# Optimization experiments

Hardware: AMD Instinct MI355X
Metric: run time of the kernel (lower is better)

The kernel has to match this reference:

```python
import jax, jax.numpy as jnp
import numpy as np

B_, N_, H_ = 4, 256, 32          # batch, nodes, neighbors (edges = B*N*H)
NC_IN, NC_OUT = 16, 16
NUM_FREQ, D_OUT, M_IN = 3, 3, 3  # degree_in = degree_out = 1 -> 2*1+1
EDGE_DIM, HID = 16, 64
LN_EPS = 1e-5


def _ln(x, gamma):
    # torch F.layer_norm over last dim, beta fixed at zero
    mu = jnp.mean(x, axis=-1, keepdims=True)
    var = jnp.var(x, axis=-1, keepdims=True)
    return (x - mu) * jax.lax.rsqrt(var + LN_EPS) * gamma


def setup_inputs() -> dict:
    key = jax.random.key(0)
    ks = jax.random.split(key, 8)

    def lin(k, fin, fout):
        lim = 1.0 / np.sqrt(fin)
        kw, kb = jax.random.split(k)
        W = jax.random.uniform(kw, (fin, fout), jnp.float32, -lim, lim)
        b = jax.random.uniform(kb, (fout,), jnp.float32, -lim, lim)
        return W, b

    W1, b1 = lin(ks[0], EDGE_DIM + 1, HID)
    W2, b2 = lin(ks[1], HID, HID)
    W3, b3 = lin(ks[2], HID, NUM_FREQ * NC_IN * NC_OUT)
    return {
        "feat": jax.random.normal(ks[3], (B_, N_, H_, EDGE_DIM + 1), jnp.float32),
        "basis": jax.random.normal(ks[4], (B_, N_, H_, D_OUT, M_IN, NUM_FREQ), jnp.float32),
        "W1": W1, "b1": b1, "g1": jnp.ones((HID,), jnp.float32),
        "W2": W2, "b2": b2, "g2": jnp.ones((HID,), jnp.float32),
        "W3": W3, "b3": b3,
    }


def reference(feat, basis, W1, b1, g1, W2, b2, g2, W3, b3):
    # radial MLP: Linear -> SiLU -> LN -> Linear -> SiLU -> LN -> Linear
    h = _ln(jax.nn.silu(feat @ W1 + b1), g1)
    h = _ln(jax.nn.silu(h @ W2 + b2), g2)
    r = h @ W3 + b3                                   # (b, n, k, o*i*f)
    R = r.reshape(*r.shape[:-1], NC_OUT, NC_IN, NUM_FREQ)  # '(o i f) -> o i f'
    # per-frequency multiply-accumulate: sum_f R[...,o,i,f] * B[...,d,m,f]
    out = jnp.einsum('bnkoif,bnkdmf->bnkodim', R, basis)   # (b,n,k,o,d,i,m)
    b, n, k = out.shape[:3]
    # contiguous reshape matches torch rearrange + view: (b,n,k, d_out*nc_out, nc_in*m_in)
    return out.reshape(b, n, k, NC_OUT * D_OUT, NC_IN * M_IN)
```

## Files before the change

kernel.cpp:

```cpp
#include <hip/hip_runtime.h>

#define E_TOTAL 32768
#define F_IN 17
#define HID 64
#define NJ 768

using bf16x8 = __attribute__((ext_vector_type(8))) short;
using f32x4  = __attribute__((ext_vector_type(4))) float;

__device__ __forceinline__ unsigned short f2bf(float x){
    unsigned u = __float_as_uint(x);
    u += 0x7fffu + ((u >> 16) & 1u);
    return (unsigned short)(u >> 16);
}

__device__ __forceinline__ float wave_sum(float x){
    x += __int_as_float(__builtin_amdgcn_update_dpp(0, __float_as_int(x), 0x111, 0xf, 0xf, true));
    x += __int_as_float(__builtin_amdgcn_update_dpp(0, __float_as_int(x), 0x112, 0xf, 0xf, true));
    x += __int_as_float(__builtin_amdgcn_update_dpp(0, __float_as_int(x), 0x114, 0xf, 0xf, true));
    x += __int_as_float(__builtin_amdgcn_update_dpp(0, __float_as_int(x), 0x118, 0xf, 0xf, true));
    x += __int_as_float(__builtin_amdgcn_update_dpp(0, __float_as_int(x), 0x142, 0xa, 0xf, true));
    x += __int_as_float(__builtin_amdgcn_update_dpp(0, __float_as_int(x), 0x143, 0xc, 0xf, true));
    return __int_as_float(__builtin_amdgcn_readlane(__float_as_int(x), 63));
}

__global__ __launch_bounds__(256) void prep_w3(const float* __restrict__ W3,
                                               unsigned short* __restrict__ w3t){
    int t = blockIdx.x * 256 + threadIdx.x;
    int n = t >> 6, k = t & 63;
    w3t[t] = f2bf(W3[k * NJ + n]);
}

__global__ __launch_bounds__(256, 3) void fused_kernel(const float* __restrict__ feat,
        const float* __restrict__ W1, const float* __restrict__ b1, const float* __restrict__ g1,
        const float* __restrict__ W2, const float* __restrict__ b2, const float* __restrict__ g2,
        const unsigned short* __restrict__ w3t, const float* __restrict__ b3,
        const float* __restrict__ basis, float* __restrict__ out){
    __shared__ __align__(16) char smem[51968];
    unsigned short* sH  = (unsigned short*)smem;
    char* rgn = smem + 2304;
    float* sW1 = (float*)rgn;
    float* sW2 = (float*)(rgn + 4352);
    float* sC  = (float*)(rgn + 20736);
    float* sFe = (float*)(rgn + 21760);
    float* sH1 = (float*)(rgn + 22848);
    float* sR  = (float*)rgn;
    float* sO  = (float*)(rgn + 12544);

    int tid = threadIdx.x;
    int e0  = blockIdx.x * 16;
    int wv = tid >> 6, l = tid & 63;
    int j = l;
    int col = l & 15, kg = l >> 4;
    int e_loc = wv * 4 + kg;
    int s = col;

    for (int i = tid; i < 272; i += 256) ((f32x4*)sW1)[i] = ((const f32x4*)W1)[i];
    #pragma unroll
    for (int k = 0; k < 4; ++k) ((f32x4*)sW2)[k * 256 + tid] = ((const f32x4*)W2)[k * 256 + tid];
    if (tid < 64){
        int g = tid >> 4, r = tid & 15;
        const float* src = (g == 0) ? b1 : (g == 1) ? g1 : (g == 2) ? b2 : g2;
        ((f32x4*)sC)[tid] = ((const f32x4*)src)[r];
    }
    if (tid < 68) ((f32x4*)sFe)[tid] = ((const f32x4*)(feat + (size_t)e0 * F_IN))[tid];
    __syncthreads();

    float acc[4], x[4];

    #pragma unroll
    for (int q = 0; q < 4; ++q) acc[q] = sC[j];
    for (int k = 0; k < F_IN; ++k){
        float w = sW1[k * 64 + j];
        #pragma unroll
        for (int q = 0; q < 4; ++q) acc[q] += sFe[(wv * 4 + q) * F_IN + k] * w;
    }
    #pragma unroll
    for (int q = 0; q < 4; ++q){
        float a = acc[q];
        float sg = 1.0f / (1.0f + __expf(-a));
        x[q] = a * sg;
        float s1 = wave_sum(x[q]);
        float s2 = wave_sum(x[q] * x[q]);
        float mu  = s1 * (1.0f / 64.0f);
        float var = s2 * (1.0f / 64.0f) - mu * mu;
        float rs  = rsqrtf(var + 1e-5f);
        sH1[(wv * 4 + q) * 64 + j] = (x[q] - mu) * rs * sC[64 + j];
    }

    #pragma unroll
    for (int q = 0; q < 4; ++q) acc[q] = sC[128 + j];
    for (int k4 = 0; k4 < 16; ++k4){
        float hv[4][4];
        #pragma unroll
        for (int q = 0; q < 4; ++q) *(float4*)hv[q] = *(const float4*)&sH1[(wv * 4 + q) * 64 + k4 * 4];
        #pragma unroll
        for (int kk = 0; kk < 4; ++kk){
            float w = sW2[(k4 * 4 + kk) * 64 + j];
            #pragma unroll
            for (int q = 0; q < 4; ++q) acc[q] += hv[q][kk] * w;
        }
    }
    #pragma unroll
    for (int q = 0; q < 4; ++q){
        float a = acc[q];
        float sg = 1.0f / (1.0f + __expf(-a));
        x[q] = a * sg;
        float s1 = wave_sum(x[q]);
        float s2 = wave_sum(x[q] * x[q]);
        float mu  = s1 * (1.0f / 64.0f);
        float var = s2 * (1.0f / 64.0f) - mu * mu;
        float rs  = rsqrtf(var + 1e-5f);
        sH[(wv * 4 + q) * 72 + j] = f2bf((x[q] - mu) * rs * sC[192 + j]);
    }

    float bs[27];
    {
        const float* bp = basis + (size_t)(e0 + e_loc) * 27;
        #pragma unroll
        for (int z = 0; z < 27; ++z) bs[z] = bp[z];
    }
    __syncthreads();

    bf16x8 a0 = *(const bf16x8*)(sH + col * 72 + kg * 8);
    bf16x8 a1 = *(const bf16x8*)(sH + col * 72 + 32 + kg * 8);

    float* outB = out + (size_t)e0 * 2304;
    const float* Rrow = sR + e_loc * 196;
    float* Orow = sO + e_loc * 580;

    for (int c4 = 0; c4 < 4; ++c4){
        if (c4 > 0){
            #pragma unroll
            for (int k = 0; k < 9; ++k){
                int idx4 = k * 256 + tid;
                int e = idx4 / 144, c = idx4 - e * 144;
                f32x4 v = *(const f32x4*)(sO + e * 580 + c * 4);
                *(f32x4*)(outB + (size_t)e * 2304 + (c4 - 1) * 576 + c * 4) = v;
            }
        }
        #pragma unroll
        for (int t = 0; t < 3; ++t){
            int n0 = c4 * 192 + wv * 48 + t * 16;
            const unsigned short* wrow = w3t + (size_t)(n0 + col) * 64;
            bf16x8 bb0 = *(const bf16x8*)(wrow + kg * 8);
            bf16x8 bb1 = *(const bf16x8*)(wrow + 32 + kg * 8);
            f32x4 acc2 = {0.f, 0.f, 0.f, 0.f};
            acc2 = __builtin_amdgcn_mfma_f32_16x16x32_bf16(a0, bb0, acc2, 0, 0, 0);
            acc2 = __builtin_amdgcn_mfma_f32_16x16x32_bf16(a1, bb1, acc2, 0, 0, 0);
            float bj = b3[n0 + col];
            int cL = wv * 48 + t * 16 + col;
            #pragma unroll
            for (int r = 0; r < 4; ++r)
                sR[(kg * 4 + r) * 196 + cL] = acc2[r] + bj;
        }
        __syncthreads();

        #pragma unroll
        for (int t2 = 0; t2 < 4; ++t2){
            const float* rp = Rrow + t2 * 48 + s * 3;
            float r0 = rp[0], r1 = rp[1], r2 = rp[2];
            #pragma unroll
            for (int d = 0; d < 3; ++d){
                float* p = Orow + t2 * 144 + d * 48 + s * 3;
                int z = d * 9;
                p[0] = r0 * bs[z + 0] + r1 * bs[z + 1] + r2 * bs[z + 2];
                p[1] = r0 * bs[z + 3] + r1 * bs[z + 4] + r2 * bs[z + 5];
                p[2] = r0 * bs[z + 6] + r1 * bs[z + 7] + r2 * bs[z + 8];
            }
        }
        __syncthreads();
    }

    #pragma unroll
    for (int k = 0; k < 9; ++k){
        int idx4 = k * 256 + tid;
        int e = idx4 / 144, c = idx4 - e * 144;
        f32x4 v = *(const f32x4*)(sO + e * 580 + c * 4);
        *(f32x4*)(outB + (size_t)e * 2304 + 3 * 576 + c * 4) = v;
    }
}

extern "C" void kernel_launch(void* const* d_in, const int* in_sizes, int n_in,
                              void* d_out, int out_size, void* d_ws, size_t ws_size,
                              hipStream_t stream) {
    const float* feat  = (const float*)d_in[0];
    const float* basis = (const float*)d_in[1];
    const float* W1 = (const float*)d_in[2];
    const float* b1 = (const float*)d_in[3];
    const float* g1 = (const float*)d_in[4];
    const float* W2 = (const float*)d_in[5];
    const float* b2 = (const float*)d_in[6];
    const float* g2 = (const float*)d_in[7];
    const float* W3 = (const float*)d_in[8];
    const float* b3 = (const float*)d_in[9];
    float* out = (float*)d_out;

    unsigned short* w3t = (unsigned short*)d_ws;

    prep_w3<<<NJ * HID / 256, 256, 0, stream>>>(W3, w3t);
    fused_kernel<<<E_TOTAL / 16, 256, 0, stream>>>(feat, W1, b1, g1, W2, b2, g2,
                                                   w3t, b3, basis, out);
}
```

Baseline: 348.9 us.

## Pad W3 frequency dim to four and write outputs directly from MFMA registers

W3 and b3 are repacked with the frequency axis padded from three to four. Each MFMA output lane then holds all three frequencies for one (o,i) pair and one edge, so the basis contraction runs in registers and writes straight to global memory. This drops the shared-memory staging of R and O, the barriers between them, and the coalesced float4 store pass. In exchange it spends a third more MFMA work on zero padding and issues scattered scalar global stores. The smaller LDS footprint also allows raising the occupancy hint to 4 blocks.

New measurement: 387.7 us. 1.11x slower.

```diff
diff --git a/kernel.cpp b/kernel.cpp
--- a/kernel.cpp
+++ b/kernel.cpp
@@ -4,6 +4,7 @@
 #define F_IN 17
 #define HID 64
 #define NJ 768
+#define NJP 1024
 
 using bf16x8 = __attribute__((ext_vector_type(8))) short;
 using f32x4  = __attribute__((ext_vector_type(4))) float;
@@ -25,35 +26,39 @@
 }
 
 __global__ __launch_bounds__(256) void prep_w3(const float* __restrict__ W3,
-                                               unsigned short* __restrict__ w3t){
+        const float* __restrict__ b3, unsigned short* __restrict__ w3tp,
+        float* __restrict__ b3p){
     int t = blockIdx.x * 256 + threadIdx.x;
-    int n = t >> 6, k = t & 63;
-    w3t[t] = f2bf(W3[k * NJ + n]);
+    if (t < NJP * HID){
+        int np = t >> 6, k = t & 63;
+        int f = np & 3, oi = np >> 2;
+        w3tp[t] = (f < 3) ? f2bf(W3[k * NJ + oi * 3 + f]) : (unsigned short)0;
+    } else if (t < NJP * HID + NJP){
+        int u = t - NJP * HID;
+        int f = u & 3, oi = u >> 2;
+        b3p[u] = (f < 3) ? b3[oi * 3 + f] : 0.0f;
+    }
 }
 
-__global__ __launch_bounds__(256, 3) void fused_kernel(const float* __restrict__ feat,
+__global__ __launch_bounds__(256, 4) void fused_kernel(const float* __restrict__ feat,
         const float* __restrict__ W1, const float* __restrict__ b1, const float* __restrict__ g1,
         const float* __restrict__ W2, const float* __restrict__ b2, const float* __restrict__ g2,
-        const unsigned short* __restrict__ w3t, const float* __restrict__ b3,
+        const unsigned short* __restrict__ w3tp, const float* __restrict__ b3p,
         const float* __restrict__ basis, float* __restrict__ out){
-    __shared__ __align__(16) char smem[51968];
-    unsigned short* sH  = (unsigned short*)smem;
+    __shared__ __align__(16) char smem[29248];
+    unsigned short* sH = (unsigned short*)smem;
     char* rgn = smem + 2304;
     float* sW1 = (float*)rgn;
     float* sW2 = (float*)(rgn + 4352);
     float* sC  = (float*)(rgn + 20736);
     float* sFe = (float*)(rgn + 21760);
     float* sH1 = (float*)(rgn + 22848);
-    float* sR  = (float*)rgn;
-    float* sO  = (float*)(rgn + 12544);
 
     int tid = threadIdx.x;
     int e0  = blockIdx.x * 16;
     int wv = tid >> 6, l = tid & 63;
     int j = l;
-    int col = l & 15, kg = l >> 4;
-    int e_loc = wv * 4 + kg;
-    int s = col;
+    int c = l & 15, kg = l >> 4;
 
     for (int i = tid; i < 272; i += 256) ((f32x4*)sW1)[i] = ((const f32x4*)W1)[i];
     #pragma unroll
@@ -116,68 +121,38 @@
 
     float bs[27];
     {
-        const float* bp = basis + (size_t)(e0 + e_loc) * 27;
+        const float* bp = basis + (size_t)(e0 + c) * 27;
         #pragma unroll
         for (int z = 0; z < 27; ++z) bs[z] = bp[z];
     }
     __syncthreads();
 
-    bf16x8 a0 = *(const bf16x8*)(sH + col * 72 + kg * 8);
-    bf16x8 a1 = *(const bf16x8*)(sH + col * 72 + 32 + kg * 8);
+    bf16x8 a0 = *(const bf16x8*)(sH + c * 72 + kg * 8);
+    bf16x8 a1 = *(const bf16x8*)(sH + c * 72 + 32 + kg * 8);
+    float* outE = out + (size_t)(e0 + c) * 2304;
 
-    float* outB = out + (size_t)e0 * 2304;
-    const float* Rrow = sR + e_loc * 196;
-    float* Orow = sO + e_loc * 580;
-
-    for (int c4 = 0; c4 < 4; ++c4){
-        if (c4 > 0){
-            #pragma unroll
-            for (int k = 0; k < 9; ++k){
-                int idx4 = k * 256 + tid;
-                int e = idx4 / 144, c = idx4 - e * 144;
-                f32x4 v = *(const f32x4*)(sO + e * 580 + c * 4);
-                *(f32x4*)(outB + (size_t)e * 2304 + (c4 - 1) * 576 + c * 4) = v;
-            }
+    #pragma unroll 4
+    for (int tt = 0; tt < 16; ++tt){
+        int tile = wv * 16 + tt;
+        const unsigned short* wr = w3tp + (size_t)(tile * 16 + c) * 64;
+        bf16x8 A0 = *(const bf16x8*)(wr + kg * 8);
+        bf16x8 A1 = *(const bf16x8*)(wr + 32 + kg * 8);
+        f32x4 ac = {0.f, 0.f, 0.f, 0.f};
+        ac = __builtin_amdgcn_mfma_f32_16x16x32_bf16(A0, a0, ac, 0, 0, 0);
+        ac = __builtin_amdgcn_mfma_f32_16x16x32_bf16(A1, a1, ac, 0, 0, 0);
+        int oi = tile * 4 + kg;
+        f32x4 bb = *(const f32x4*)(b3p + oi * 4);
+        float r0 = ac[0] + bb[0];
+        float r1 = ac[1] + bb[1];
+        float r2 = ac[2] + bb[2];
+        float* p = outE + (oi >> 4) * 144 + (oi & 15) * 3;
+        #pragma unroll
+        for (int d = 0; d < 3; ++d){
+            int z = d * 9;
+            p[d * 48 + 0] = r0 * bs[z + 0] + r1 * bs[z + 1] + r2 * bs[z + 2];
+            p[d * 48 + 1] = r0 * bs[z + 3] + r1 * bs[z + 4] + r2 * bs[z + 5];
+            p[d * 48 + 2] = r0 * bs[z + 6] + r1 * bs[z + 7] + r2 * bs[z + 8];
         }
-        #pragma unroll
-        for (int t = 0; t < 3; ++t){
-            int n0 = c4 * 192 + wv * 48 + t * 16;
-            const unsigned short* wrow = w3t + (size_t)(n0 + col) * 64;
-            bf16x8 bb0 = *(const bf16x8*)(wrow + kg * 8);
-            bf16x8 bb1 = *(const bf16x8*)(wrow + 32 + kg * 8);
-            f32x4 acc2 = {0.f, 0.f, 0.f, 0.f};
-            acc2 = __builtin_amdgcn_mfma_f32_16x16x32_bf16(a0, bb0, acc2, 0, 0, 0);
-            acc2 = __builtin_amdgcn_mfma_f32_16x16x32_bf16(a1, bb1, acc2, 0, 0, 0);
-            float bj = b3[n0 + col];
-            int cL = wv * 48 + t * 16 + col;
-            #pragma unroll
-            for (int r = 0; r < 4; ++r)
-                sR[(kg * 4 + r) * 196 + cL] = acc2[r] + bj;
-        }
-        __syncthreads();
-
-        #pragma unroll
-        for (int t2 = 0; t2 < 4; ++t2){
-            const float* rp = Rrow + t2 * 48 + s * 3;
-            float r0 = rp[0], r1 = rp[1], r2 = rp[2];
-            #pragma unroll
-            for (int d = 0; d < 3; ++d){
-                float* p = Orow + t2 * 144 + d * 48 + s * 3;
-                int z = d * 9;
-                p[0] = r0 * bs[z + 0] + r1 * bs[z + 1] + r2 * bs[z + 2];
-                p[1] = r0 * bs[z + 3] + r1 * bs[z + 4] + r2 * bs[z + 5];
-                p[2] = r0 * bs[z + 6] + r1 * bs[z + 7] + r2 * bs[z + 8];
-            }
-        }
-        __syncthreads();
-    }
-
-    #pragma unroll
-    for (int k = 0; k < 9; ++k){
-        int idx4 = k * 256 + tid;
-        int e = idx4 / 144, c = idx4 - e * 144;
-        f32x4 v = *(const f32x4*)(sO + e * 580 + c * 4);
-        *(f32x4*)(outB + (size_t)e * 2304 + 3 * 576 + c * 4) = v;
     }
 }
 
@@ -196,9 +171,10 @@
     const float* b3 = (const float*)d_in[9];
     float* out = (float*)d_out;
 
-    unsigned short* w3t = (unsigned short*)d_ws;
+    unsigned short* w3tp = (unsigned short*)d_ws;
+    float* b3p = (float*)(w3tp + (size_t)NJP * HID);
 
-    prep_w3<<<NJ * HID / 256, 256, 0, stream>>>(W3, w3t);
+    prep_w3<<<(NJP * HID + NJP + 255) / 256, 256, 0, stream>>>(W3, b3, w3tp, b3p);
     fused_kernel<<<E_TOTAL / 16, 256, 0, stream>>>(feat, W1, b1, g1, W2, b2, g2,
-                                                   w3t, b3, basis, out);
+                                                   w3tp, b3p, basis, out);
 }
```
